# Optimization experiments

Hardware: AMD Instinct MI355X
Metric: run time of the kernel (lower is better)

Reference implementation:

```python
import jax, jax.numpy as jnp
import numpy as np

WS = 7          # window_size
HEADS = 3
HD = 32         # head_dim
HIDDEN = 96
DISP = WS // 2  # 3
NEG_INF = float('-inf')


def _relative_indices():
    idx = np.array([[i, j] for i in range(WS) for j in range(WS)])
    rel = idx[None, :, :] - idx[:, None, :] + WS - 1  # [49,49,2], values in [0, 2*WS-2]
    return rel.astype(np.int32)


def _upper_lower_mask():
    m = np.zeros((WS * WS, WS * WS), dtype=np.float32)
    m[-DISP * WS:, :-DISP * WS] = NEG_INF
    m[:-DISP * WS, -DISP * WS:] = NEG_INF
    return m


def setup_inputs() -> dict:
    key = jax.random.key(0)
    ks = jax.random.split(key, 6)
    B, H, W = 32, 56, 56
    inner = HEADS * HD
    return {
        'x': jax.random.normal(ks[0], (B, H, W, HIDDEN), jnp.float32),
        'w_qkv': jax.random.normal(ks[1], (HIDDEN, inner * 3), jnp.float32) * 0.05,
        'b_qkv': jax.random.normal(ks[2], (inner * 3,), jnp.float32) * 0.05,
        'pos_embedding': jax.random.normal(ks[3], (2 * WS - 1, 2 * WS - 1), jnp.float32),
        'w_out': jax.random.normal(ks[4], (inner, HIDDEN), jnp.float32) * 0.05,
        'b_out': jax.random.normal(ks[5], (HIDDEN,), jnp.float32) * 0.05,
    }


def reference(x, w_qkv, b_qkv, pos_embedding, w_out, b_out):
    B, H, W, _ = x.shape
    nw_h, nw_w = H // WS, W // WS
    nw = nw_h * nw_w
    scale = HIDDEN ** (-0.5)  # original scales by hidden_dim**-0.5

    rel = jnp.asarray(_relative_indices())
    ul_mask = jnp.asarray(_upper_lower_mask())

    # cyclic shift
    xs = jnp.roll(x, (-DISP, -DISP), axis=(1, 2))
    qkv = xs @ w_qkv + b_qkv
    q, k, v = jnp.split(qkv, 3, axis=-1)

    def to_windows(e):
        # [B,H,W,heads*hd] -> [B,heads,nw,WS*WS,hd]
        e = e.reshape(B, nw_h, WS, nw_w, WS, HEADS, HD)
        e = e.transpose(0, 5, 1, 3, 2, 4, 6)
        return e.reshape(B, HEADS, nw, WS * WS, HD)

    q, k, v = to_windows(q), to_windows(k), to_windows(v)

    att = jnp.einsum('bhwid,bhwjd->bhwij', q, k) * scale
    att = att + pos_embedding[rel[:, :, 0], rel[:, :, 1]]
    # shifted: original only adds upper_lower_mask (right_left line is a no-op bug)
    att = att.at[:, :, -nw_w:].add(ul_mask)
    att = jax.nn.softmax(att, axis=-1)

    out = jnp.einsum('bhwij,bhwjd->bhwid', att, v)
    out = out.reshape(B, HEADS, nw_h, nw_w, WS, WS, HD)
    out = out.transpose(0, 2, 4, 3, 5, 1, 6).reshape(B, H, W, HEADS * HD)
    out = out @ w_out + b_out
    out = jnp.roll(out, (DISP, DISP), axis=(1, 2))
    return out
```

## Files before the change

kernel.cpp:

```cpp
#include <hip/hip_runtime.h>
#include <hip/hip_bf16.h>

using bf16 = __hip_bfloat16;
typedef __attribute__((ext_vector_type(8))) short short8;
typedef __attribute__((ext_vector_type(4))) float floatx4;

#define B_      32
#define HH      56
#define WW      56
#define HIDDEN  96
#define HEADS   3
#define HD      32
#define WS_     7
#define DISP    3
#define NWH     8
#define NWW     8
#define NW      64
#define WS2     49
#define NFRAG_QKV (3*6*3*64)
#define NFRAG_OUT (6*3*64)
#define NPEL      (2*64*64)

__device__ inline unsigned short bf16_bits(float f) {
  unsigned u = __float_as_uint(f);
  unsigned r = u + 0x7fffu + ((u >> 16) & 1u);
  return (unsigned short)(r >> 16);
}
__device__ inline unsigned packbf(float lo, float hi) {
  return (unsigned)bf16_bits(lo) | ((unsigned)bf16_bits(hi) << 16);
}

__global__ __launch_bounds__(256) void prep_kernel(
    const float* __restrict__ w_qkv, const float* __restrict__ w_out,
    const float* __restrict__ pos_emb,
    bf16* __restrict__ wfq, bf16* __restrict__ wfo, float* __restrict__ pelT) {
  int f = blockIdx.x * 256 + threadIdx.x;
  if (f < NFRAG_QKV) {
    int lane = f & 63, t = f >> 6;
    int kb = t % 3, t2 = t / 3, c6 = t2 % 6, ci = t2 / 6;
    int col = ci * 96 + c6 * 16 + (lane & 15);
    int k0 = kb * 32 + (lane >> 4) * 8;
    bf16 vals[8];
#pragma unroll
    for (int j = 0; j < 8; j++) vals[j] = __float2bfloat16(w_qkv[(k0 + j) * 288 + col]);
    *(short8*)&wfq[(size_t)f * 8] = *(const short8*)vals;
  } else if (f < NFRAG_QKV + NFRAG_OUT) {
    int fo = f - NFRAG_QKV;
    int lane = fo & 63, t = fo >> 6;
    int kb = t % 3, c6 = t / 3;
    int col = c6 * 16 + (lane & 15);
    int k0 = kb * 32 + (lane >> 4) * 8;
    bf16 vals[8];
#pragma unroll
    for (int j = 0; j < 8; j++) vals[j] = __float2bfloat16(w_out[(k0 + j) * 96 + col]);
    *(short8*)&wfo[(size_t)fo * 8] = *(const short8*)vals;
  } else {
    int p = f - (NFRAG_QKV + NFRAG_OUT);
    if (p < NPEL) {
      int mk = p >> 12, i = (p >> 6) & 63, j = p & 63;
      int iy = i / WS_, ix = i % WS_, jy = j / WS_, jx = j % WS_;
      int idx = (jy - iy + 6) * 13 + (jx - ix + 6);
      idx = idx < 0 ? 0 : (idx > 168 ? 168 : idx);
      bool live = (i < WS2) && (j < WS2) && !(mk && ((i >= 28) != (j >= 28)));
      pelT[p] = live ? pos_emb[idx] : -1e30f;
    }
  }
}

__global__ __launch_bounds__(256, 4) void fused_swin_kernel(
    const float* __restrict__ x,
    const bf16* __restrict__ wfq, const bf16* __restrict__ wfo,
    const float* __restrict__ b_qkv, const float* __restrict__ b_out,
    const float* __restrict__ pelT, float* __restrict__ out) {

  __shared__ unsigned short slabA[3][64][32];
  __shared__ unsigned short slabB[3][64][32];
  __shared__ unsigned short vT[3][32][72];

  const int blk = blockIdx.x;
  const int nw = blk & 63, b = blk >> 6;
  const int wy = nw >> 3, wx = nw & 7;
  const int tid = threadIdx.x;
  const int lane = tid & 63, wv = tid >> 6;
  const int n_ = lane & 15, quad = lane >> 4;

  const short8* wfQ = (const short8*)wfq;
  short8 wcur0 = wfQ[(size_t)((wv * 3 + 0) * 64 + lane)];
  short8 wcur1 = wfQ[(size_t)((wv * 3 + 1) * 64 + lane)];
  short8 wcur2 = wfQ[(size_t)((wv * 3 + 2) * 64 + lane)];

  {
    const int rowp = tid >> 2, s0 = tid & 3;
    const bool haveRow = rowp < WS2;
    const float* xrow = x;
    if (haveRow) {
      const int py = rowp / WS_, px = rowp % WS_;
      int h = wy * WS_ + py + DISP; if (h >= HH) h -= HH;
      int w = wx * WS_ + px + DISP; if (w >= WW) w -= WW;
      xrow = &x[((size_t)(b * HH + h) * WW + w) * HIDDEN];
    }
#pragma unroll
    for (int p = 0; p < 6; p++) {
      const int seg = s0 + 4 * p;
      const int kb = seg >> 3, c4 = (seg & 7) << 2;
      uint2 pk = (uint2){0u, 0u};
      if (haveRow) {
        const float4 xv = *(const float4*)&xrow[seg * 4];
        pk.x = packbf(xv.x, xv.y);
        pk.y = packbf(xv.z, xv.w);
      }
      *(uint2*)&slabA[kb][rowp][c4] = pk;
    }
  }

  const bool maskedw = (nw >= NW - NWW);
  float pelv[4][4];
  {
    const float4* pt4 = (const float4*)&pelT[(maskedw ? 4096 : 0) + (16 * wv + n_) * 64];
#pragma unroll
    for (int jt = 0; jt < 4; jt++) {
      const float4 p4 = pt4[8 * (jt & 1) + (jt >> 1) + 2 * quad];
      pelv[jt][0] = p4.x; pelv[jt][1] = p4.y;
      pelv[jt][2] = p4.z; pelv[jt][3] = p4.w;
    }
  }
  __syncthreads();

  short8 af[4][3];
#pragma unroll
  for (int m = 0; m < 4; m++)
#pragma unroll
    for (int kb = 0; kb < 3; kb++)
      af[m][kb] = *(const short8*)&slabA[kb][16 * m + n_][quad * 8];
  __syncthreads();

  {
    const int rB = 32 * ((n_ >> 2) & 1) + 4 * (n_ >> 3) + (n_ & 3);
    int t = wv;
    while (t < 18) {
      const int tn = t + 4;
      short8 wn0 = wcur0, wn1 = wcur1, wn2 = wcur2;
      if (tn < 18) {
        wn0 = wfQ[(size_t)((tn * 3 + 0) * 64 + lane)];
        wn1 = wfQ[(size_t)((tn * 3 + 1) * 64 + lane)];
        wn2 = wfQ[(size_t)((tn * 3 + 2) * 64 + lane)];
      }
      const int ci = t / 6, c6 = t % 6, head = c6 >> 1;
      floatx4 acc[4];
      if (ci < 2) {
        const float4 bq = *(const float4*)&b_qkv[t * 16 + 4 * quad];
#pragma unroll
        for (int m = 0; m < 4; m++) acc[m] = (floatx4){bq.x, bq.y, bq.z, bq.w};
#pragma unroll
        for (int m = 0; m < 4; m++) {
          acc[m] = __builtin_amdgcn_mfma_f32_16x16x32_bf16(wcur0, af[m][0], acc[m], 0, 0, 0);
          acc[m] = __builtin_amdgcn_mfma_f32_16x16x32_bf16(wcur1, af[m][1], acc[m], 0, 0, 0);
          acc[m] = __builtin_amdgcn_mfma_f32_16x16x32_bf16(wcur2, af[m][2], acc[m], 0, 0, 0);
        }
        const int dc0 = ((c6 & 1) << 4) + 4 * quad;
        if (ci == 0) {
#pragma unroll
          for (int m = 0; m < 4; m++) {
            uint2 st;
            st.x = packbf(acc[m][0], acc[m][1]);
            st.y = packbf(acc[m][2], acc[m][3]);
            *(uint2*)&slabA[head][16 * m + n_][dc0] = st;
          }
        } else {
#pragma unroll
          for (int m = 0; m < 4; m++) {
            uint2 st;
            st.x = packbf(acc[m][0], acc[m][1]);
            st.y = packbf(acc[m][2], acc[m][3]);
            *(uint2*)&slabB[head][rB + 8 * m][dc0] = st;
          }
        }
      } else {
        const float bias = b_qkv[t * 16 + n_];
#pragma unroll
        for (int m = 0; m < 4; m++) acc[m] = (floatx4){bias, bias, bias, bias};
#pragma unroll
        for (int m = 0; m < 4; m++) {
          acc[m] = __builtin_amdgcn_mfma_f32_16x16x32_bf16(af[m][0], wcur0, acc[m], 0, 0, 0);
          acc[m] = __builtin_amdgcn_mfma_f32_16x16x32_bf16(af[m][1], wcur1, acc[m], 0, 0, 0);
          acc[m] = __builtin_amdgcn_mfma_f32_16x16x32_bf16(af[m][2], wcur2, acc[m], 0, 0, 0);
        }
        const int dc = ((c6 & 1) << 4) + n_;
#pragma unroll
        for (int m = 0; m < 4; m++) {
          uint2 st;
          st.x = packbf(acc[m][0], acc[m][1]);
          st.y = packbf(acc[m][2], acc[m][3]);
          *(uint2*)&vT[head][dc][16 * m + 4 * quad] = st;
        }
      }
      wcur0 = wn0; wcur1 = wn1; wcur2 = wn2;
      t = tn;
    }
  }
  __syncthreads();

  const float scale = 0.10206207261596575f;
  const floatx4 zero4 = (floatx4){0.f, 0.f, 0.f, 0.f};
#pragma unroll
  for (int h = 0; h < HEADS; h++) {
    const short8 aq = *(const short8*)&slabA[h][16 * wv + n_][quad * 8];
    floatx4 sAcc[4];
#pragma unroll
    for (int jt = 0; jt < 4; jt++) {
      const short8 bk = *(const short8*)&slabB[h][16 * jt + n_][quad * 8];
      sAcc[jt] = __builtin_amdgcn_mfma_f32_16x16x32_bf16(bk, aq, zero4, 0, 0, 0);
    }

    float ei[4][4];
    float s = 0.f;
#pragma unroll
    for (int jt = 0; jt < 4; jt++)
#pragma unroll
      for (int r = 0; r < 4; r++) {
        const float e = __expf(fmaf(sAcc[jt][r], scale, pelv[jt][r]));
        ei[jt][r] = e;
        s += e;
      }
    s += __shfl_xor(s, 16);
    s += __shfl_xor(s, 32);
    const float invq = s > 0.f ? 1.0f / s : 0.f;

    unsigned pk2[4][2];
#pragma unroll
    for (int jt = 0; jt < 4; jt++) {
      pk2[jt][0] = packbf(ei[jt][0], ei[jt][1]);
      pk2[jt][1] = packbf(ei[jt][2], ei[jt][3]);
    }
    short8 apf[2];
#pragma unroll
    for (int kc = 0; kc < 2; kc++) {
      union { unsigned u[4]; short8 s8; } fu;
      fu.u[0] = pk2[kc][0];
      fu.u[1] = pk2[kc][1];
      fu.u[2] = pk2[2 + kc][0];
      fu.u[3] = pk2[2 + kc][1];
      apf[kc] = fu.s8;
    }

    floatx4 oAcc[2] = {zero4, zero4};
#pragma unroll
    for (int nt = 0; nt < 2; nt++)
#pragma unroll
      for (int kc = 0; kc < 2; kc++) {
        const short8 bv = *(const short8*)&vT[h][16 * nt + n_][32 * kc + quad * 8];
        oAcc[nt] = __builtin_amdgcn_mfma_f32_16x16x32_bf16(bv, apf[kc], oAcc[nt], 0, 0, 0);
      }
#pragma unroll
    for (int nt = 0; nt < 2; nt++) {
      uint2 st;
      st.x = packbf(oAcc[nt][0] * invq, oAcc[nt][1] * invq);
      st.y = packbf(oAcc[nt][2] * invq, oAcc[nt][3] * invq);
      *(uint2*)&slabA[h][16 * wv + n_][16 * nt + 4 * quad] = st;
    }
  }
  __syncthreads();

  short8 af2[4][3];
#pragma unroll
  for (int m = 0; m < 4; m++)
#pragma unroll
    for (int kb = 0; kb < 3; kb++)
      af2[m][kb] = *(const short8*)&slabA[kb][16 * m + n_][quad * 8];

  unsigned obase[4][4];
#pragma unroll
  for (int m = 0; m < 4; m++)
#pragma unroll
    for (int r = 0; r < 4; r++) {
      const int row = 16 * m + 4 * quad + r;
      const int py = row / WS_, px = row % WS_;
      int hg = wy * WS_ + py + DISP; if (hg >= HH) hg -= HH;
      int wg = wx * WS_ + px + DISP; if (wg >= WW) wg -= WW;
      obase[m][r] = (unsigned)(((b * HH + hg) * WW + wg) * HIDDEN + n_);
    }

  const short8* wfO = (const short8*)wfo;
  {
    int t = wv;
    short8 oc0 = wfO[(size_t)((t * 3 + 0) * 64 + lane)];
    short8 oc1 = wfO[(size_t)((t * 3 + 1) * 64 + lane)];
    short8 oc2 = wfO[(size_t)((t * 3 + 2) * 64 + lane)];
    while (t < 6) {
      const int tn = t + 4;
      short8 on0 = oc0, on1 = oc1, on2 = oc2;
      if (tn < 6) {
        on0 = wfO[(size_t)((tn * 3 + 0) * 64 + lane)];
        on1 = wfO[(size_t)((tn * 3 + 1) * 64 + lane)];
        on2 = wfO[(size_t)((tn * 3 + 2) * 64 + lane)];
      }
      const float bias = b_out[t * 16 + n_];
      floatx4 acc[4];
#pragma unroll
      for (int m = 0; m < 4; m++) acc[m] = (floatx4){bias, bias, bias, bias};
#pragma unroll
      for (int m = 0; m < 4; m++) {
        acc[m] = __builtin_amdgcn_mfma_f32_16x16x32_bf16(af2[m][0], oc0, acc[m], 0, 0, 0);
        acc[m] = __builtin_amdgcn_mfma_f32_16x16x32_bf16(af2[m][1], oc1, acc[m], 0, 0, 0);
        acc[m] = __builtin_amdgcn_mfma_f32_16x16x32_bf16(af2[m][2], oc2, acc[m], 0, 0, 0);
      }
#pragma unroll
      for (int m = 0; m < 4; m++)
#pragma unroll
        for (int r = 0; r < 4; r++) {
          if (16 * m + 4 * quad + r < WS2)
            out[(size_t)obase[m][r] + t * 16] = acc[m][r];
        }
      oc0 = on0; oc1 = on1; oc2 = on2;
      t = tn;
    }
  }
}

extern "C" void kernel_launch(void* const* d_in, const int* in_sizes, int n_in,
                              void* d_out, int out_size, void* d_ws, size_t ws_size,
                              hipStream_t stream) {
  const float* x     = (const float*)d_in[0];
  const float* w_qkv = (const float*)d_in[1];
  const float* b_qkv = (const float*)d_in[2];
  const float* pos   = (const float*)d_in[3];
  const float* w_out = (const float*)d_in[4];
  const float* b_out = (const float*)d_in[5];
  float* out = (float*)d_out;

  bf16* wfq = (bf16*)d_ws;
  bf16* wfo = wfq + (size_t)NFRAG_QKV * 8;
  float* pelT = (float*)((char*)d_ws + (size_t)(NFRAG_QKV + NFRAG_OUT) * 8 * 2);

  prep_kernel<<<50, 256, 0, stream>>>(w_qkv, w_out, pos, wfq, wfo, pelT);
  fused_swin_kernel<<<B_ * NW, 256, 0, stream>>>(x, wfq, wfo, b_qkv, b_out, pelT, out);
}
```

Before: 126.5 us.

## Swizzle LDS slabs, use hardware bf16 pack, rcp, and MFMA priority hints

XOR-swizzles the 64-byte rows of the slabA/slabB shared-memory tiles by row to reduce LDS bank conflicts on short8 fragment reads. Replaces the software round-to-nearest bf16 packing with the v_cvt_pk_bf16_f32 instruction, and the softmax division with a fast reciprocal. Wraps the attention MFMA loops in s_setprio to favour matrix issue. The swizzle must match on every reader and writer, and the fast reciprocal slightly changes rounding.

```diff
diff --git a/kernel.cpp b/kernel.cpp
--- a/kernel.cpp
+++ b/kernel.cpp
@@ -26,8 +26,15 @@
   unsigned r = u + 0x7fffu + ((u >> 16) & 1u);
   return (unsigned short)(r >> 16);
 }
-__device__ inline unsigned packbf(float lo, float hi) {
-  return (unsigned)bf16_bits(lo) | ((unsigned)bf16_bits(hi) << 16);
+
+__device__ inline unsigned cvtpk(float lo, float hi) {
+  unsigned r;
+  asm("v_cvt_pk_bf16_f32 %0, %1, %2" : "=v"(r) : "v"(lo), "v"(hi));
+  return r;
+}
+
+__device__ inline unsigned short* swz(const unsigned short* plane, int row, int boff) {
+  return (unsigned short*)((char*)plane + (row << 6) + (boff ^ ((row & 3) << 4)));
 }
 
 __global__ __launch_bounds__(256) void prep_kernel(
@@ -102,14 +109,14 @@
 #pragma unroll
     for (int p = 0; p < 6; p++) {
       const int seg = s0 + 4 * p;
-      const int kb = seg >> 3, c4 = (seg & 7) << 2;
+      const int kb = seg >> 3;
       uint2 pk = (uint2){0u, 0u};
       if (haveRow) {
         const float4 xv = *(const float4*)&xrow[seg * 4];
-        pk.x = packbf(xv.x, xv.y);
-        pk.y = packbf(xv.z, xv.w);
-      }
-      *(uint2*)&slabA[kb][rowp][c4] = pk;
+        pk.x = cvtpk(xv.x, xv.y);
+        pk.y = cvtpk(xv.z, xv.w);
+      }
+      *(uint2*)swz(&slabA[kb][0][0], rowp, (seg & 7) * 8) = pk;
     }
   }
 
@@ -131,7 +138,7 @@
   for (int m = 0; m < 4; m++)
 #pragma unroll
     for (int kb = 0; kb < 3; kb++)
-      af[m][kb] = *(const short8*)&slabA[kb][16 * m + n_][quad * 8];
+      af[m][kb] = *(const short8*)swz(&slabA[kb][0][0], 16 * m + n_, quad * 16);
   __syncthreads();
 
   {
@@ -157,22 +164,22 @@
           acc[m] = __builtin_amdgcn_mfma_f32_16x16x32_bf16(wcur1, af[m][1], acc[m], 0, 0, 0);
           acc[m] = __builtin_amdgcn_mfma_f32_16x16x32_bf16(wcur2, af[m][2], acc[m], 0, 0, 0);
         }
-        const int dc0 = ((c6 & 1) << 4) + 4 * quad;
+        const int boff = ((c6 & 1) << 5) + quad * 8;
         if (ci == 0) {
 #pragma unroll
           for (int m = 0; m < 4; m++) {
             uint2 st;
-            st.x = packbf(acc[m][0], acc[m][1]);
-            st.y = packbf(acc[m][2], acc[m][3]);
-            *(uint2*)&slabA[head][16 * m + n_][dc0] = st;
+            st.x = cvtpk(acc[m][0], acc[m][1]);
+            st.y = cvtpk(acc[m][2], acc[m][3]);
+            *(uint2*)swz(&slabA[head][0][0], 16 * m + n_, boff) = st;
           }
         } else {
 #pragma unroll
           for (int m = 0; m < 4; m++) {
             uint2 st;
-            st.x = packbf(acc[m][0], acc[m][1]);
-            st.y = packbf(acc[m][2], acc[m][3]);
-            *(uint2*)&slabB[head][rB + 8 * m][dc0] = st;
+            st.x = cvtpk(acc[m][0], acc[m][1]);
+            st.y = cvtpk(acc[m][2], acc[m][3]);
+            *(uint2*)swz(&slabB[head][0][0], rB + 8 * m, boff) = st;
           }
         }
       } else {
@@ -189,8 +196,8 @@
 #pragma unroll
         for (int m = 0; m < 4; m++) {
           uint2 st;
-          st.x = packbf(acc[m][0], acc[m][1]);
-          st.y = packbf(acc[m][2], acc[m][3]);
+          st.x = cvtpk(acc[m][0], acc[m][1]);
+          st.y = cvtpk(acc[m][2], acc[m][3]);
           *(uint2*)&vT[head][dc][16 * m + 4 * quad] = st;
         }
       }
@@ -204,13 +211,15 @@
   const floatx4 zero4 = (floatx4){0.f, 0.f, 0.f, 0.f};
 #pragma unroll
   for (int h = 0; h < HEADS; h++) {
-    const short8 aq = *(const short8*)&slabA[h][16 * wv + n_][quad * 8];
+    const short8 aq = *(const short8*)swz(&slabA[h][0][0], 16 * wv + n_, quad * 16);
     floatx4 sAcc[4];
+    __builtin_amdgcn_s_setprio(1);
 #pragma unroll
     for (int jt = 0; jt < 4; jt++) {
-      const short8 bk = *(const short8*)&slabB[h][16 * jt + n_][quad * 8];
+      const short8 bk = *(const short8*)swz(&slabB[h][0][0], 16 * jt + n_, quad * 16);
       sAcc[jt] = __builtin_amdgcn_mfma_f32_16x16x32_bf16(bk, aq, zero4, 0, 0, 0);
     }
+    __builtin_amdgcn_s_setprio(0);
 
     float ei[4][4];
     float s = 0.f;
@@ -224,13 +233,13 @@
       }
     s += __shfl_xor(s, 16);
     s += __shfl_xor(s, 32);
-    const float invq = s > 0.f ? 1.0f / s : 0.f;
+    const float invq = s > 0.f ? __builtin_amdgcn_rcpf(s) : 0.f;
 
     unsigned pk2[4][2];
 #pragma unroll
     for (int jt = 0; jt < 4; jt++) {
-      pk2[jt][0] = packbf(ei[jt][0], ei[jt][1]);
-      pk2[jt][1] = packbf(ei[jt][2], ei[jt][3]);
+      pk2[jt][0] = cvtpk(ei[jt][0], ei[jt][1]);
+      pk2[jt][1] = cvtpk(ei[jt][2], ei[jt][3]);
     }
     short8 apf[2];
 #pragma unroll
@@ -244,6 +253,7 @@
     }
 
     floatx4 oAcc[2] = {zero4, zero4};
+    __builtin_amdgcn_s_setprio(1);
 #pragma unroll
     for (int nt = 0; nt < 2; nt++)
 #pragma unroll
@@ -251,12 +261,13 @@
         const short8 bv = *(const short8*)&vT[h][16 * nt + n_][32 * kc + quad * 8];
         oAcc[nt] = __builtin_amdgcn_mfma_f32_16x16x32_bf16(bv, apf[kc], oAcc[nt], 0, 0, 0);
       }
+    __builtin_amdgcn_s_setprio(0);
 #pragma unroll
     for (int nt = 0; nt < 2; nt++) {
       uint2 st;
-      st.x = packbf(oAcc[nt][0] * invq, oAcc[nt][1] * invq);
-      st.y = packbf(oAcc[nt][2] * invq, oAcc[nt][3] * invq);
-      *(uint2*)&slabA[h][16 * wv + n_][16 * nt + 4 * quad] = st;
+      st.x = cvtpk(oAcc[nt][0] * invq, oAcc[nt][1] * invq);
+      st.y = cvtpk(oAcc[nt][2] * invq, oAcc[nt][3] * invq);
+      *(uint2*)swz(&slabA[h][0][0], 16 * wv + n_, nt * 32 + quad * 8) = st;
     }
   }
   __syncthreads();
@@ -266,7 +277,7 @@
   for (int m = 0; m < 4; m++)
 #pragma unroll
     for (int kb = 0; kb < 3; kb++)
-      af2[m][kb] = *(const short8*)&slabA[kb][16 * m + n_][quad * 8];
+      af2[m][kb] = *(const short8*)swz(&slabA[kb][0][0], 16 * m + n_, quad * 16);
 
   unsigned obase[4][4];
 #pragma unroll
```

Result: faster. 121.3 us (-4.1%).
